# Kernel tuning notes

Hardware: AMD Instinct MI355X
Metric: run time of the kernel (lower is better)

Reference implementation:

```python
import jax, jax.numpy as jnp
import numpy as np

HEADS = 8
EPS = 1e-5
PW1 = (512, 8, 14, 14)   # (C, T, H, W), C = headsize1 * heads
PW2 = (512, 32, 7, 7)


def _ln(x, g, b):
    m = jnp.mean(x, axis=-1, keepdims=True)
    v = jnp.var(x, axis=-1, keepdims=True)
    return (x - m) * jax.lax.rsqrt(v + EPS) * g + b


def _mha(q, k, v):
    b, nq, c = q.shape
    nk = k.shape[1]
    hd = c // HEADS
    qh = q.reshape(b, nq, HEADS, hd).transpose(0, 2, 1, 3)  # [b,h,nq,hd]
    kh = k.reshape(b, nk, HEADS, hd).transpose(0, 2, 1, 3)
    vh = v.reshape(b, nk, HEADS, hd).transpose(0, 2, 1, 3)
    s = jnp.einsum('bhqd,bhkd->bhqk', qh, kh) * (hd ** -0.5)
    a = jax.nn.softmax(s, axis=-1)
    o = jnp.einsum('bhqk,bhkd->bhqd', a, vh)
    return o.transpose(0, 2, 1, 3).reshape(b, nq, c)


def _tok(x):
    b, c, t, h, w = x.shape
    return x.transpose(0, 2, 3, 4, 1).reshape(b, t * h * w, c)


def _detok(t, c, T, H, W):
    b = t.shape[0]
    return t.reshape(b, T, H, W, c).transpose(0, 4, 1, 2, 3)


def _out_head(y, w, bias, bn_g, bn_b):
    # 1x1x1 Conv3d + ReLU + BatchNorm3d (eval, running mean 0 / var 1)
    z = jnp.einsum('bcthw,oc->bothw', y, w) + bias[None, :, None, None, None]
    z = jax.nn.relu(z)
    z = z * jax.lax.rsqrt(jnp.float32(1.0 + EPS))
    return z * bn_g[None, :, None, None, None] + bn_b[None, :, None, None, None]


def reference(x1, x2, Wq1, bq1, Wk1, bk1, Wv1, bv1, ln1_g, ln1_b,
              Wq2, bq2, Wk2, bk2, Wv2, bv2, ln2_g, ln2_b,
              out1_w, out1_b, bn1_g, bn1_b, out2_w, out2_b, bn2_g, bn2_b):
    t1 = _tok(x1)  # [B, 1568, 512]
    t2 = _tok(x2)  # [B, 1568, 512]
    for i in range(3):  # three chained norm + cross-attn stages
        q1 = _ln(t1, ln1_g[i], ln1_b[i]) @ Wq1[i].T + bq1[i]
        k1 = t2 @ Wk1[i].T + bk1[i]
        v1 = t2 @ Wv1[i].T + bv1[i]
        q2 = _ln(t2, ln2_g[i], ln2_b[i]) @ Wq2[i].T + bq2[i]
        k2 = t1 @ Wk2[i].T + bk2[i]
        v2 = t1 @ Wv2[i].T + bv2[i]
        t1 = t1 + _mha(q1, k1, v1)
        t2 = t2 + _mha(q2, k2, v2)
    y1 = _detok(t1, *PW1)
    y2 = _detok(t2, *PW2)
    z1 = _out_head(y1, out1_w, out1_b, bn1_g, bn1_b)
    z2 = _out_head(y2, out2_w, out2_b, bn2_g, bn2_b)
    return (z1, z2)


def setup_inputs() -> dict:
    key = jax.random.key(0)
    ks = jax.random.split(key, 12)
    C = 512
    w = lambda k, shp: jax.random.normal(k, shp, jnp.float32) * 0.02
    return {
        'x1': jax.random.normal(ks[0], (4, C, 8, 14, 14), jnp.float32),
        'x2': jax.random.normal(ks[1], (4, C, 32, 7, 7), jnp.float32),
        'Wq1': w(ks[2], (3, C, C)), 'bq1': jnp.zeros((3, C), jnp.float32),
        'Wk1': w(ks[3], (3, C, C)), 'bk1': jnp.zeros((3, C), jnp.float32),
        'Wv1': w(ks[4], (3, C, C)), 'bv1': jnp.zeros((3, C), jnp.float32),
        'ln1_g': jnp.ones((3, C), jnp.float32), 'ln1_b': jnp.zeros((3, C), jnp.float32),
        'Wq2': w(ks[5], (3, C, C)), 'bq2': jnp.zeros((3, C), jnp.float32),
        'Wk2': w(ks[6], (3, C, C)), 'bk2': jnp.zeros((3, C), jnp.float32),
        'Wv2': w(ks[7], (3, C, C)), 'bv2': jnp.zeros((3, C), jnp.float32),
        'ln2_g': jnp.ones((3, C), jnp.float32), 'ln2_b': jnp.zeros((3, C), jnp.float32),
        'out1_w': w(ks[8], (C, C)), 'out1_b': jnp.zeros((C,), jnp.float32),
        'bn1_g': jnp.ones((C,), jnp.float32), 'bn1_b': jnp.zeros((C,), jnp.float32),
        'out2_w': w(ks[9], (C, C)), 'out2_b': jnp.zeros((C,), jnp.float32),
        'bn2_g': jnp.ones((C,), jnp.float32), 'bn2_b': jnp.zeros((C,), jnp.float32),
    }
```

## Files before the change

kernel.cpp:

```cpp
#include <hip/hip_runtime.h>

typedef __bf16 bf16_t;
typedef __bf16 bf16x8 __attribute__((ext_vector_type(8)));
typedef __bf16 bf16x4 __attribute__((ext_vector_type(4)));
typedef float f32x4 __attribute__((ext_vector_type(4)));
typedef float f32x16 __attribute__((ext_vector_type(16)));
typedef unsigned u32x4 __attribute__((ext_vector_type(4)));

#define NTOK 1568
#define CDIM 512
#define BATCH 4
#define MROWS (BATCH*NTOK)
#define RSQ1PEPS 0.9999950000374997f
#define CEXP 0.1803368801111204f
#define DEFER_THR 44.3614195558365f

__device__ __forceinline__ float fexp2(float x) {
  float r;
  asm("v_exp_f32 %0, %1" : "=v"(r) : "v"(x));
  return r;
}

struct CastArgs { const float* s[20]; };
__global__ __launch_bounds__(256) void cast_kernel(CastArgs ca, bf16_t* __restrict__ out) {
  int idx = blockIdx.x * 256 + threadIdx.x;
  int m = idx >> 16;
  const float4* sp = (const float4*)ca.s[m];
  float4 v = sp[idx & 65535];
  bf16x4 o;
  o[0] = (bf16_t)v.x; o[1] = (bf16_t)v.y; o[2] = (bf16_t)v.z; o[3] = (bf16_t)v.w;
  *(bf16x4*)(out + (size_t)idx * 4) = o;
}

struct TokArgs { const float* x[2]; float* tf[2]; bf16_t* tb[2]; };
__global__ __launch_bounds__(256) void tok_kernel(TokArgs ta) {
  __shared__ float tile[32][33];
  int z = blockIdx.z, sel = z >> 2, b = z & 3;
  int c0 = blockIdx.y * 32, s0 = blockIdx.x * 32;
  int tx = threadIdx.x, ty = threadIdx.y;
  const float* xp = ta.x[sel] + (size_t)b * CDIM * NTOK;
  for (int r = 0; r < 32; r += 8)
    tile[ty + r][tx] = xp[(size_t)(c0 + ty + r) * NTOK + s0 + tx];
  __syncthreads();
  float* tfp = ta.tf[sel] + (size_t)b * NTOK * CDIM;
  bf16_t* tbp = ta.tb[sel] + (size_t)b * NTOK * CDIM;
  for (int r = 0; r < 32; r += 8) {
    float v = tile[tx][ty + r];
    size_t idx = (size_t)(s0 + ty + r) * CDIM + c0 + tx;
    tfp[idx] = v;
    tbp[idx] = (bf16_t)v;
  }
}

__global__ __launch_bounds__(64) void ln_kernel(
    const float* __restrict__ t1, const float* __restrict__ t2,
    const float* __restrict__ g1, const float* __restrict__ b1,
    const float* __restrict__ g2, const float* __restrict__ b2,
    bf16_t* __restrict__ o1, bf16_t* __restrict__ o2) {
  int row = blockIdx.x;
  const float* t; const float* g; const float* bt; bf16_t* out;
  if (row < MROWS) { t = t1; g = g1; bt = b1; out = o1; }
  else { row -= MROWS; t = t2; g = g2; bt = b2; out = o2; }
  int l = threadIdx.x;
  const float* x = t + (size_t)row * CDIM;
  float4 v0 = ((const float4*)x)[l];
  float4 v1 = ((const float4*)x)[l + 64];
  float s = v0.x + v0.y + v0.z + v0.w + v1.x + v1.y + v1.z + v1.w;
  float sq = v0.x*v0.x + v0.y*v0.y + v0.z*v0.z + v0.w*v0.w
           + v1.x*v1.x + v1.y*v1.y + v1.z*v1.z + v1.w*v1.w;
  for (int m = 1; m < 64; m <<= 1) { s += __shfl_xor(s, m); sq += __shfl_xor(sq, m); }
  float mean = s * (1.f / 512.f);
  float var = sq * (1.f / 512.f) - mean * mean;
  float rs = rsqrtf(var + 1e-5f);
  float4 g0 = ((const float4*)g)[l], g1v = ((const float4*)g)[l + 64];
  float4 b0 = ((const float4*)bt)[l], b1v = ((const float4*)bt)[l + 64];
  bf16x4 o0, o1v;
  o0[0] = (bf16_t)((v0.x - mean) * rs * g0.x + b0.x);
  o0[1] = (bf16_t)((v0.y - mean) * rs * g0.y + b0.y);
  o0[2] = (bf16_t)((v0.z - mean) * rs * g0.z + b0.z);
  o0[3] = (bf16_t)((v0.w - mean) * rs * g0.w + b0.w);
  o1v[0] = (bf16_t)((v1.x - mean) * rs * g1v.x + b1v.x);
  o1v[1] = (bf16_t)((v1.y - mean) * rs * g1v.y + b1v.y);
  o1v[2] = (bf16_t)((v1.z - mean) * rs * g1v.z + b1v.z);
  o1v[3] = (bf16_t)((v1.w - mean) * rs * g1v.w + b1v.w);
  *(bf16x4*)(out + (size_t)row * CDIM + l * 4) = o0;
  *(bf16x4*)(out + (size_t)row * CDIM + 256 + l * 4) = o1v;
}

template<int MODE>
__device__ __forceinline__ void gemm_core(
    bf16_t (* __restrict__ As)[40], bf16_t (* __restrict__ Bs)[40],
    const bf16_t* __restrict__ A, const bf16_t* __restrict__ Bp,
    const float* __restrict__ bias, const float* __restrict__ bng,
    const float* __restrict__ bnb, bf16_t* __restrict__ outb,
    float* __restrict__ outf, int m0, int n0, int Nvalid) {
  int tid = threadIdx.x;
  int w = tid >> 6, l = tid & 63, lr = l & 15, kg = l >> 4;
  int wm = (w >> 1) * 64, wn = (w & 1) * 64;
  f32x4 acc[4][4];
  for (int i = 0; i < 4; i++)
    for (int j = 0; j < 4; j++)
      acc[i][j] = f32x4{0.f, 0.f, 0.f, 0.f};
  int srow = tid >> 1;
  int soff = (tid & 1) * 16;
  int brow = n0 + srow;
  if (MODE != 0 && brow >= Nvalid) brow = Nvalid - 1;
  const bf16_t* aq = A + (size_t)(m0 + srow) * CDIM + soff;
  const bf16_t* bq = Bp + (size_t)brow * CDIM + soff;
  for (int kk = 0; kk < 16; kk++) {
    __syncthreads();
    bf16x8 a0 = *(const bf16x8*)(aq);
    bf16x8 a1 = *(const bf16x8*)(aq + 8);
    bf16x8 b0 = *(const bf16x8*)(bq);
    bf16x8 b1 = *(const bf16x8*)(bq + 8);
    aq += 32; bq += 32;
    *(bf16x8*)&As[srow][soff] = a0;
    *(bf16x8*)&As[srow][soff + 8] = a1;
    *(bf16x8*)&Bs[srow][soff] = b0;
    *(bf16x8*)&Bs[srow][soff + 8] = b1;
    __syncthreads();
    bf16x8 af[4], bfr[4];
    for (int i = 0; i < 4; i++) af[i] = *(const bf16x8*)&As[wm + i * 16 + lr][kg * 8];
    for (int j = 0; j < 4; j++) bfr[j] = *(const bf16x8*)&Bs[wn + j * 16 + lr][kg * 8];
    for (int i = 0; i < 4; i++)
      for (int j = 0; j < 4; j++)
        acc[i][j] = __builtin_amdgcn_mfma_f32_16x16x32_bf16(af[i], bfr[j], acc[i][j], 0, 0, 0);
  }
  for (int i = 0; i < 4; i++)
    for (int j = 0; j < 4; j++) {
      int rbase = m0 + wm + i * 16 + kg * 4;
      int col = n0 + wn + j * 16 + lr;
      for (int r = 0; r < 4; r++) {
        int row = rbase + r;
        float v = acc[i][j][r];
        if (MODE == 0) {
          v += bias[col];
          outb[(size_t)row * CDIM + col] = (bf16_t)v;
        } else if (MODE == 1) {
          v += bias[row];
          v = v > 0.f ? v : 0.f;
          v *= RSQ1PEPS;
          v = v * bng[row] + bnb[row];
          if (col < Nvalid) outf[(size_t)row * NTOK + col] = v;
        } else {
          v += bias[row];
          if (col < Nvalid) outb[(size_t)row * NTOK + col] = (bf16_t)v;
        }
      }
    }
}

struct ProjArgs {
  const bf16_t* A0[4]; const bf16_t* W0[4]; const float* b0[4]; bf16_t* o0[4];
  const bf16_t* W2[2]; const bf16_t* B2[2]; const float* b2[2]; bf16_t* o2[2];
};
__global__ __launch_bounds__(256) void proj_kernel(ProjArgs p) {
  __shared__ bf16_t As[128][40];
  __shared__ bf16_t Bs[128][40];
  int id = blockIdx.x;
  if (id < 784) {
    int set = id / 196, rem = id % 196;
    int n0 = (rem & 3) * 128, m0 = (rem >> 2) * 128;
    gemm_core<0>(As, Bs, p.A0[set], p.W0[set], p.b0[set], nullptr, nullptr,
                 p.o0[set], nullptr, m0, n0, 512);
  } else {
    int j = id - 784;
    int unit = j / 52;
    int which = unit >> 2, bat = unit & 3;
    int rem = j % 52;
    int n0 = (rem % 13) * 128, m0 = (rem / 13) * 128;
    gemm_core<2>(As, Bs, p.W2[which], p.B2[which] + (size_t)bat * NTOK * CDIM,
                 p.b2[which], nullptr, nullptr,
                 p.o2[which] + (size_t)bat * CDIM * NTOK, nullptr, m0, n0, NTOK);
  }
}

__global__ __launch_bounds__(256) void head_kernel(
    const bf16_t* __restrict__ W1, const bf16_t* __restrict__ W2,
    const bf16_t* __restrict__ t1b, const bf16_t* __restrict__ t2b,
    const float* __restrict__ b1, const float* __restrict__ b2,
    const float* __restrict__ bng1, const float* __restrict__ bnb1,
    const float* __restrict__ bng2, const float* __restrict__ bnb2,
    float* __restrict__ out) {
  __shared__ bf16_t As[128][40];
  __shared__ bf16_t Bs[128][40];
  int z = blockIdx.z;
  int which = z >> 2, bat = z & 3;
  const bf16_t* A = which ? W2 : W1;
  const bf16_t* Bp = (which ? t2b : t1b) + (size_t)bat * NTOK * CDIM;
  const float* bias = which ? b2 : b1;
  const float* bng = which ? bng2 : bng1;
  const float* bnb = which ? bnb2 : bnb1;
  float* outf = out + (size_t)which * BATCH * CDIM * NTOK + (size_t)bat * CDIM * NTOK;
  int m0 = blockIdx.y * 128, n0 = blockIdx.x * 128;
  gemm_core<1>(As, Bs, A, Bp, bias, bng, bnb, nullptr, outf, m0, n0, NTOK);
}

__device__ __forceinline__ void attn_tile(
    const bf16_t* __restrict__ Ksl, const bf16_t* __restrict__ Vsl,
    const bf16x8* __restrict__ qf, int lo, int hi,
    float& m_i, float& l_i, f32x16& ot0, f32x16& ot1) {
  f32x16 st;
#pragma unroll
  for (int r = 0; r < 16; r++) st[r] = 0.f;
  __builtin_amdgcn_s_setprio(1);
#pragma unroll
  for (int c = 0; c < 4; c++) {
    bf16x8 kf = *(const bf16x8*)(Ksl + lo * 64 + ((c * 16 + hi * 8) ^ ((lo & 7) << 3)));
    st = __builtin_amdgcn_mfma_f32_32x32x16_bf16(kf, qf[c], st, 0, 0, 0);
  }
  __builtin_amdgcn_s_setprio(0);
  float a0 = fmaxf(st[0], st[1]), a1 = fmaxf(st[2], st[3]);
  float a2 = fmaxf(st[4], st[5]), a3 = fmaxf(st[6], st[7]);
  float a4 = fmaxf(st[8], st[9]), a5 = fmaxf(st[10], st[11]);
  float a6 = fmaxf(st[12], st[13]), a7 = fmaxf(st[14], st[15]);
  a0 = fmaxf(a0, a1); a2 = fmaxf(a2, a3); a4 = fmaxf(a4, a5); a6 = fmaxf(a6, a7);
  a0 = fmaxf(a0, a2); a4 = fmaxf(a4, a6);
  float tm = fmaxf(a0, a4);
  tm = fmaxf(tm, __shfl_xor(tm, 32));
  if (!__all(tm <= m_i + DEFER_THR)) {
    float mn = fmaxf(m_i, tm);
    float alpha = fexp2((m_i - mn) * CEXP);
#pragma unroll
    for (int r = 0; r < 16; r++) { ot0[r] *= alpha; ot1[r] *= alpha; }
    l_i *= alpha;
    m_i = mn;
  }
  float nmC = -m_i * CEXP;
  float p[16];
#pragma unroll
  for (int r = 0; r < 16; r++) p[r] = fexp2(fmaf(st[r], CEXP, nmC));
  float s0 = (p[0] + p[1]) + (p[2] + p[3]);
  float s1 = (p[4] + p[5]) + (p[6] + p[7]);
  float s2 = (p[8] + p[9]) + (p[10] + p[11]);
  float s3 = (p[12] + p[13]) + (p[14] + p[15]);
  float ts = (s0 + s1) + (s2 + s3);
  ts += __shfl_xor(ts, 32);
  l_i += ts;
  unsigned pk[8];
#pragma unroll
  for (int g = 0; g < 8; g++) {
    union { bf16_t hh[2]; unsigned u; } cv;
    cv.hh[0] = (bf16_t)p[2 * g];
    cv.hh[1] = (bf16_t)p[2 * g + 1];
    pk[g] = cv.u;
  }
  unsigned x0 = __shfl_xor((int)pk[0], 32), x1 = __shfl_xor((int)pk[1], 32);
  unsigned x2 = __shfl_xor((int)pk[2], 32), x3 = __shfl_xor((int)pk[3], 32);
  unsigned x4 = __shfl_xor((int)pk[4], 32), x5 = __shfl_xor((int)pk[5], 32);
  unsigned x6 = __shfl_xor((int)pk[6], 32), x7 = __shfl_xor((int)pk[7], 32);
  union { u32x4 u; bf16x8 bv; } F0, F1;
  F0.u[0] = hi ? x2 : pk[0];
  F0.u[1] = hi ? x3 : pk[1];
  F0.u[2] = hi ? pk[2] : x0;
  F0.u[3] = hi ? pk[3] : x1;
  F1.u[0] = hi ? x6 : pk[4];
  F1.u[1] = hi ? x7 : pk[5];
  F1.u[2] = hi ? pk[6] : x4;
  F1.u[3] = hi ? pk[7] : x5;
  __builtin_amdgcn_s_setprio(1);
  {
    bf16x8 v0 = *(const bf16x8*)(Vsl + lo * 40 + hi * 8);
    ot0 = __builtin_amdgcn_mfma_f32_32x32x16_bf16(v0, F0.bv, ot0, 0, 0, 0);
    bf16x8 v1 = *(const bf16x8*)(Vsl + lo * 40 + 16 + hi * 8);
    ot0 = __builtin_amdgcn_mfma_f32_32x32x16_bf16(v1, F1.bv, ot0, 0, 0, 0);
    bf16x8 v2 = *(const bf16x8*)(Vsl + (32 + lo) * 40 + hi * 8);
    ot1 = __builtin_amdgcn_mfma_f32_32x32x16_bf16(v2, F0.bv, ot1, 0, 0, 0);
    bf16x8 v3 = *(const bf16x8*)(Vsl + (32 + lo) * 40 + 16 + hi * 8);
    ot1 = __builtin_amdgcn_mfma_f32_32x32x16_bf16(v3, F1.bv, ot1, 0, 0, 0);
  }
  __builtin_amdgcn_s_setprio(0);
}

struct AttnArgs {
  const bf16_t* q[2]; const bf16_t* k[2]; const bf16_t* v[2];
  float* tf[2]; bf16_t* tb[2];
};

#define ATTN_STEP(TT, CUR, WSLOT, ISLOT, VLOAD, VSTORE)                              \
  {                                                                                  \
    int ktn = (TT) + 2 > 48 ? 48 : (TT) + 2;                                         \
    __builtin_amdgcn_global_load_lds(                                                \
        (const __attribute__((address_space(1))) unsigned*)(kgl + (size_t)ktn * 32 * CDIM), \
        (__attribute__((address_space(3))) unsigned*)&Ks[ISLOT][w * 8][0], 16, 0, 0); \
    VLOAD = *(const bf16x8*)(vgl + ktn * 32);                                        \
    attn_tile(&Ks[CUR][0][0], &Vs[CUR][0][0], qf, lo, hi, m_i, l_i, ot0, ot1);       \
    asm volatile("s_waitcnt vmcnt(2)" ::: "memory");                                 \
    *(bf16x8*)&Vs[WSLOT][vd][vc] = VSTORE;                                           \
    asm volatile("s_waitcnt lgkmcnt(0)\n\ts_barrier" ::: "memory");                  \
  }

__global__ __launch_bounds__(256) void attn_kernel(AttnArgs aa) {
  __shared__ alignas(16) bf16_t Ks[4][32][64];
  __shared__ alignas(16) bf16_t Vs[4][64][40];
  int id = blockIdx.x;
  int xcd = id & 7, sl = id >> 3;
  int g = xcd + ((sl / 13) << 3);
  int qt = sl % 13;
  int ss = g >> 5, b = (g >> 3) & 3, h = g & 7;
  const bf16_t* qg = aa.q[ss];
  const bf16_t* kgp = aa.k[ss];
  const bf16_t* vtg = aa.v[ss];
  float* tf = aa.tf[ss];
  bf16_t* tb = aa.tb[ss];
  int tid = threadIdx.x, w = tid >> 6, l = tid & 63;
  int lo = l & 31, hi = l >> 5;
  const size_t kbase = ((size_t)b * NTOK) * CDIM + h * 64;
  const size_t vbase = ((size_t)b * CDIM + h * 64) * NTOK;

  int q0 = qt * 128 + w * 32;
  int qrow = q0 + lo;
  int qr = qrow < NTOK ? qrow : NTOK - 1;
  const bf16_t* qp = qg + kbase + (size_t)qr * CDIM + hi * 8;
  bf16x8 qf[4];
  qf[0] = *(const bf16x8*)(qp);
  qf[1] = *(const bf16x8*)(qp + 16);
  qf[2] = *(const bf16x8*)(qp + 32);
  qf[3] = *(const bf16x8*)(qp + 48);
  asm volatile("" : "+v"(qf[0]), "+v"(qf[1]), "+v"(qf[2]), "+v"(qf[3]));
  asm volatile("s_waitcnt vmcnt(0)" ::: "memory");

  int ksr = w * 8 + (l >> 3);
  int ksc = 8 * ((l & 7) ^ ((l >> 3) & 7));
  const bf16_t* kgl = kgp + kbase + (size_t)ksr * CDIM + ksc;
  int vd = tid >> 2, vc = (tid & 3) * 8;
  const bf16_t* vgl = vtg + vbase + (size_t)vd * NTOK + vc;

  float m_i = -3.0e38f, l_i = 0.f;
  f32x16 ot0, ot1;
#pragma unroll
  for (int r = 0; r < 16; r++) { ot0[r] = 0.f; ot1[r] = 0.f; }

  bf16x8 vrA, vrB;
  __builtin_amdgcn_global_load_lds(
      (const __attribute__((address_space(1))) unsigned*)(kgl),
      (__attribute__((address_space(3))) unsigned*)&Ks[0][w * 8][0], 16, 0, 0);
  vrB = *(const bf16x8*)(vgl);
  __builtin_amdgcn_global_load_lds(
      (const __attribute__((address_space(1))) unsigned*)(kgl + (size_t)32 * CDIM),
      (__attribute__((address_space(3))) unsigned*)&Ks[1][w * 8][0], 16, 0, 0);
  vrA = *(const bf16x8*)(vgl + 32);
  asm volatile("s_waitcnt vmcnt(2)" ::: "memory");
  *(bf16x8*)&Vs[0][vd][vc] = vrB;
  asm volatile("s_waitcnt lgkmcnt(0)\n\ts_barrier" ::: "memory");

  for (int t = 0; t < 48; t += 4) {
    ATTN_STEP(t + 0, 0, 1, 2, vrB, vrA);
    ATTN_STEP(t + 1, 1, 2, 3, vrA, vrB);
    ATTN_STEP(t + 2, 2, 3, 0, vrB, vrA);
    ATTN_STEP(t + 3, 3, 0, 1, vrA, vrB);
  }
  attn_tile(&Ks[0][0][0], &Vs[0][0][0], qf, lo, hi, m_i, l_i, ot0, ot1);
  asm volatile("s_waitcnt vmcnt(0)" ::: "memory");

  if (qrow < NTOK) {
    float inv = 1.f / l_i;
    float* tfp = tf + ((size_t)b * NTOK + qrow) * CDIM + h * 64 + hi * 4;
    bf16_t* tbp = tb + ((size_t)b * NTOK + qrow) * CDIM + h * 64 + hi * 4;
#pragma unroll
    for (int db = 0; db < 2; db++) {
#pragma unroll
      for (int gq = 0; gq < 4; gq++) {
        int doff = db * 32 + gq * 8;
        float4 old = *(float4*)(tfp + doff);
        float4 nv;
        float a0 = (db ? ot1[gq * 4 + 0] : ot0[gq * 4 + 0]) * inv;
        float a1 = (db ? ot1[gq * 4 + 1] : ot0[gq * 4 + 1]) * inv;
        float a2 = (db ? ot1[gq * 4 + 2] : ot0[gq * 4 + 2]) * inv;
        float a3 = (db ? ot1[gq * 4 + 3] : ot0[gq * 4 + 3]) * inv;
        nv.x = old.x + a0; nv.y = old.y + a1; nv.z = old.z + a2; nv.w = old.w + a3;
        *(float4*)(tfp + doff) = nv;
        bf16x4 ob;
        ob[0] = (bf16_t)nv.x; ob[1] = (bf16_t)nv.y;
        ob[2] = (bf16_t)nv.z; ob[3] = (bf16_t)nv.w;
        *(bf16x4*)(tbp + doff) = ob;
      }
    }
  }
}

extern "C" void kernel_launch(void* const* d_in, const int* in_sizes, int n_in,
                              void* d_out, int out_size, void* d_ws, size_t ws_size,
                              hipStream_t stream) {
  (void)in_sizes; (void)n_in; (void)out_size; (void)ws_size;
  const float* x1 = (const float*)d_in[0];
  const float* x2 = (const float*)d_in[1];
  const float* Wq1 = (const float*)d_in[2];
  const float* bq1 = (const float*)d_in[3];
  const float* Wk1 = (const float*)d_in[4];
  const float* bk1 = (const float*)d_in[5];
  const float* Wv1 = (const float*)d_in[6];
  const float* bv1 = (const float*)d_in[7];
  const float* ln1_g = (const float*)d_in[8];
  const float* ln1_b = (const float*)d_in[9];
  const float* Wq2 = (const float*)d_in[10];
  const float* bq2 = (const float*)d_in[11];
  const float* Wk2 = (const float*)d_in[12];
  const float* bk2 = (const float*)d_in[13];
  const float* Wv2 = (const float*)d_in[14];
  const float* bv2 = (const float*)d_in[15];
  const float* ln2_g = (const float*)d_in[16];
  const float* ln2_b = (const float*)d_in[17];
  const float* out1_w = (const float*)d_in[18];
  const float* out1_b = (const float*)d_in[19];
  const float* bn1_g = (const float*)d_in[20];
  const float* bn1_b = (const float*)d_in[21];
  const float* out2_w = (const float*)d_in[22];
  const float* out2_b = (const float*)d_in[23];
  const float* bn2_g = (const float*)d_in[24];
  const float* bn2_b = (const float*)d_in[25];

  const size_t WMAT = 512 * 512;
  char* ws = (char*)d_ws;
  bf16_t* wb = (bf16_t*)ws;
  size_t off = 20 * WMAT * sizeof(bf16_t);
  float* t1f = (float*)(ws + off); off += (size_t)MROWS * CDIM * 4;
  float* t2f = (float*)(ws + off); off += (size_t)MROWS * CDIM * 4;
  bf16_t* t1b = (bf16_t*)(ws + off); off += (size_t)MROWS * CDIM * 2;
  bf16_t* t2b = (bf16_t*)(ws + off); off += (size_t)MROWS * CDIM * 2;
  bf16_t* l1b = (bf16_t*)(ws + off); off += (size_t)MROWS * CDIM * 2;
  bf16_t* l2b = (bf16_t*)(ws + off); off += (size_t)MROWS * CDIM * 2;
  bf16_t* q1b = (bf16_t*)(ws + off); off += (size_t)MROWS * CDIM * 2;
  bf16_t* k1b = (bf16_t*)(ws + off); off += (size_t)MROWS * CDIM * 2;
  bf16_t* v1b = (bf16_t*)(ws + off); off += (size_t)MROWS * CDIM * 2;
  bf16_t* q2b = (bf16_t*)(ws + off); off += (size_t)MROWS * CDIM * 2;
  bf16_t* k2b = (bf16_t*)(ws + off); off += (size_t)MROWS * CDIM * 2;
  bf16_t* v2b = (bf16_t*)(ws + off); off += (size_t)MROWS * CDIM * 2;

  CastArgs ca;
  for (int i = 0; i < 3; i++) {
    ca.s[0 + i] = Wq1 + (size_t)i * WMAT;
    ca.s[3 + i] = Wk1 + (size_t)i * WMAT;
    ca.s[6 + i] = Wv1 + (size_t)i * WMAT;
    ca.s[9 + i] = Wq2 + (size_t)i * WMAT;
    ca.s[12 + i] = Wk2 + (size_t)i * WMAT;
    ca.s[15 + i] = Wv2 + (size_t)i * WMAT;
  }
  ca.s[18] = out1_w;
  ca.s[19] = out2_w;
  cast_kernel<<<5120, 256, 0, stream>>>(ca, wb);

  TokArgs ta;
  ta.x[0] = x1; ta.x[1] = x2;
  ta.tf[0] = t1f; ta.tf[1] = t2f;
  ta.tb[0] = t1b; ta.tb[1] = t2b;
  tok_kernel<<<dim3(49, 16, 8), dim3(32, 8), 0, stream>>>(ta);

  AttnArgs aa;
  aa.q[0] = q1b; aa.q[1] = q2b;
  aa.k[0] = k1b; aa.k[1] = k2b;
  aa.v[0] = v1b; aa.v[1] = v2b;
  aa.tf[0] = t1f; aa.tf[1] = t2f;
  aa.tb[0] = t1b; aa.tb[1] = t2b;

  for (int i = 0; i < 3; i++) {
    ln_kernel<<<2 * MROWS, 64, 0, stream>>>(t1f, t2f,
        ln1_g + i * 512, ln1_b + i * 512, ln2_g + i * 512, ln2_b + i * 512,
        l1b, l2b);
    ProjArgs pa;
    pa.A0[0] = l1b; pa.W0[0] = wb + (0 + i) * WMAT; pa.b0[0] = bq1 + i * 512; pa.o0[0] = q1b;
    pa.A0[1] = t2b; pa.W0[1] = wb + (3 + i) * WMAT; pa.b0[1] = bk1 + i * 512; pa.o0[1] = k1b;
    pa.A0[2] = l2b; pa.W0[2] = wb + (9 + i) * WMAT; pa.b0[2] = bq2 + i * 512; pa.o0[2] = q2b;
    pa.A0[3] = t1b; pa.W0[3] = wb + (12 + i) * WMAT; pa.b0[3] = bk2 + i * 512; pa.o0[3] = k2b;
    pa.W2[0] = wb + (6 + i) * WMAT; pa.B2[0] = t2b; pa.b2[0] = bv1 + i * 512; pa.o2[0] = v1b;
    pa.W2[1] = wb + (15 + i) * WMAT; pa.B2[1] = t1b; pa.b2[1] = bv2 + i * 512; pa.o2[1] = v2b;
    proj_kernel<<<1200, 256, 0, stream>>>(pa);
    attn_kernel<<<832, 256, 0, stream>>>(aa);
  }

  float* out = (float*)d_out;
  head_kernel<<<dim3(13, 4, 8), 256, 0, stream>>>(
      wb + 18 * WMAT, wb + 19 * WMAT, t1b, t2b,
      out1_b, out2_b, bn1_g, bn1_b, bn2_g, bn2_b, out);
}
```

Measured before the change: 487.4 us.

## Process 64-key attention tiles with triple-buffered direct-to-LDS K and V loads

The attention inner loop now handles 64 keys per step instead of 32, halving the number of barriers and pipeline steps, and uses a 3-slot ring buffer in place of 4 slots. V is now loaded straight into LDS with global_load_lds and an XOR swizzle, removing the register staging and separate LDS store. The cross-half P fragment exchange uses v_permlane32_swap in place of eight shuffles. The cost is more live registers per step (two score accumulators) and a special tail tile.

```diff
diff --git a/kernel.cpp b/kernel.cpp
--- a/kernel.cpp
+++ b/kernel.cpp
@@ -19,6 +19,12 @@
   float r;
   asm("v_exp_f32 %0, %1" : "=v"(r) : "v"(x));
   return r;
+}
+
+__device__ __forceinline__ void glds16(const bf16_t* src, bf16_t* dst) {
+  __builtin_amdgcn_global_load_lds(
+      (const __attribute__((address_space(1))) unsigned*)src,
+      (__attribute__((address_space(3))) unsigned*)dst, 16, 0, 0);
 }
 
 struct CastArgs { const float* s[20]; };
@@ -196,47 +202,16 @@
   gemm_core<1>(As, Bs, A, Bp, bias, bng, bnb, nullptr, outf, m0, n0, NTOK);
 }
 
-__device__ __forceinline__ void attn_tile(
-    const bf16_t* __restrict__ Ksl, const bf16_t* __restrict__ Vsl,
-    const bf16x8* __restrict__ qf, int lo, int hi,
-    float& m_i, float& l_i, f32x16& ot0, f32x16& ot1) {
-  f32x16 st;
-#pragma unroll
-  for (int r = 0; r < 16; r++) st[r] = 0.f;
-  __builtin_amdgcn_s_setprio(1);
-#pragma unroll
-  for (int c = 0; c < 4; c++) {
-    bf16x8 kf = *(const bf16x8*)(Ksl + lo * 64 + ((c * 16 + hi * 8) ^ ((lo & 7) << 3)));
-    st = __builtin_amdgcn_mfma_f32_32x32x16_bf16(kf, qf[c], st, 0, 0, 0);
-  }
-  __builtin_amdgcn_s_setprio(0);
-  float a0 = fmaxf(st[0], st[1]), a1 = fmaxf(st[2], st[3]);
-  float a2 = fmaxf(st[4], st[5]), a3 = fmaxf(st[6], st[7]);
-  float a4 = fmaxf(st[8], st[9]), a5 = fmaxf(st[10], st[11]);
-  float a6 = fmaxf(st[12], st[13]), a7 = fmaxf(st[14], st[15]);
+__device__ __forceinline__ float tree_max16(const f32x16& s) {
+  float a0 = fmaxf(s[0], s[1]), a1 = fmaxf(s[2], s[3]);
+  float a2 = fmaxf(s[4], s[5]), a3 = fmaxf(s[6], s[7]);
+  float a4 = fmaxf(s[8], s[9]), a5 = fmaxf(s[10], s[11]);
+  float a6 = fmaxf(s[12], s[13]), a7 = fmaxf(s[14], s[15]);
   a0 = fmaxf(a0, a1); a2 = fmaxf(a2, a3); a4 = fmaxf(a4, a5); a6 = fmaxf(a6, a7);
-  a0 = fmaxf(a0, a2); a4 = fmaxf(a4, a6);
-  float tm = fmaxf(a0, a4);
-  tm = fmaxf(tm, __shfl_xor(tm, 32));
-  if (!__all(tm <= m_i + DEFER_THR)) {
-    float mn = fmaxf(m_i, tm);
-    float alpha = fexp2((m_i - mn) * CEXP);
-#pragma unroll
-    for (int r = 0; r < 16; r++) { ot0[r] *= alpha; ot1[r] *= alpha; }
-    l_i *= alpha;
-    m_i = mn;
-  }
-  float nmC = -m_i * CEXP;
-  float p[16];
-#pragma unroll
-  for (int r = 0; r < 16; r++) p[r] = fexp2(fmaf(st[r], CEXP, nmC));
-  float s0 = (p[0] + p[1]) + (p[2] + p[3]);
-  float s1 = (p[4] + p[5]) + (p[6] + p[7]);
-  float s2 = (p[8] + p[9]) + (p[10] + p[11]);
-  float s3 = (p[12] + p[13]) + (p[14] + p[15]);
-  float ts = (s0 + s1) + (s2 + s3);
-  ts += __shfl_xor(ts, 32);
-  l_i += ts;
+  return fmaxf(fmaxf(a0, a2), fmaxf(a4, a6));
+}
+
+__device__ __forceinline__ void build_frags(const float* p, bf16x8& Fa, bf16x8& Fb) {
   unsigned pk[8];
 #pragma unroll
   for (int g = 0; g < 8; g++) {
@@ -245,29 +220,101 @@
     cv.hh[1] = (bf16_t)p[2 * g + 1];
     pk[g] = cv.u;
   }
-  unsigned x0 = __shfl_xor((int)pk[0], 32), x1 = __shfl_xor((int)pk[1], 32);
-  unsigned x2 = __shfl_xor((int)pk[2], 32), x3 = __shfl_xor((int)pk[3], 32);
-  unsigned x4 = __shfl_xor((int)pk[4], 32), x5 = __shfl_xor((int)pk[5], 32);
-  unsigned x6 = __shfl_xor((int)pk[6], 32), x7 = __shfl_xor((int)pk[7], 32);
-  union { u32x4 u; bf16x8 bv; } F0, F1;
-  F0.u[0] = hi ? x2 : pk[0];
-  F0.u[1] = hi ? x3 : pk[1];
-  F0.u[2] = hi ? pk[2] : x0;
-  F0.u[3] = hi ? pk[3] : x1;
-  F1.u[0] = hi ? x6 : pk[4];
-  F1.u[1] = hi ? x7 : pk[5];
-  F1.u[2] = hi ? pk[6] : x4;
-  F1.u[3] = hi ? pk[7] : x5;
+  asm volatile("v_permlane32_swap_b32 %0, %1" : "+v"(pk[0]), "+v"(pk[2]));
+  asm volatile("v_permlane32_swap_b32 %0, %1" : "+v"(pk[1]), "+v"(pk[3]));
+  asm volatile("v_permlane32_swap_b32 %0, %1" : "+v"(pk[4]), "+v"(pk[6]));
+  asm volatile("v_permlane32_swap_b32 %0, %1" : "+v"(pk[5]), "+v"(pk[7]));
+  union { u32x4 u; bf16x8 bv; } A, B;
+  A.u[0] = pk[0]; A.u[1] = pk[1]; A.u[2] = pk[2]; A.u[3] = pk[3];
+  B.u[0] = pk[4]; B.u[1] = pk[5]; B.u[2] = pk[6]; B.u[3] = pk[7];
+  Fa = A.bv; Fb = B.bv;
+}
+
+template<bool TAIL>
+__device__ __forceinline__ void attn_tile64(
+    const bf16_t* __restrict__ Ksl, const bf16_t* __restrict__ Vsl,
+    const bf16x8* __restrict__ qf, const f32x16& z, int lo, int hi,
+    float& m_i, float& l_i, f32x16& ot0, f32x16& ot1) {
+  int sw = (lo & 7) << 3;
+  f32x16 sa, sb;
   __builtin_amdgcn_s_setprio(1);
   {
-    bf16x8 v0 = *(const bf16x8*)(Vsl + lo * 40 + hi * 8);
-    ot0 = __builtin_amdgcn_mfma_f32_32x32x16_bf16(v0, F0.bv, ot0, 0, 0, 0);
-    bf16x8 v1 = *(const bf16x8*)(Vsl + lo * 40 + 16 + hi * 8);
-    ot0 = __builtin_amdgcn_mfma_f32_32x32x16_bf16(v1, F1.bv, ot0, 0, 0, 0);
-    bf16x8 v2 = *(const bf16x8*)(Vsl + (32 + lo) * 40 + hi * 8);
-    ot1 = __builtin_amdgcn_mfma_f32_32x32x16_bf16(v2, F0.bv, ot1, 0, 0, 0);
-    bf16x8 v3 = *(const bf16x8*)(Vsl + (32 + lo) * 40 + 16 + hi * 8);
-    ot1 = __builtin_amdgcn_mfma_f32_32x32x16_bf16(v3, F1.bv, ot1, 0, 0, 0);
+    const bf16_t* kr = Ksl + lo * 64;
+    bf16x8 k0 = *(const bf16x8*)(kr + ((hi * 8) ^ sw));
+    sa = __builtin_amdgcn_mfma_f32_32x32x16_bf16(k0, qf[0], z, 0, 0, 0);
+    bf16x8 k1 = *(const bf16x8*)(kr + ((16 + hi * 8) ^ sw));
+    sa = __builtin_amdgcn_mfma_f32_32x32x16_bf16(k1, qf[1], sa, 0, 0, 0);
+    bf16x8 k2 = *(const bf16x8*)(kr + ((32 + hi * 8) ^ sw));
+    sa = __builtin_amdgcn_mfma_f32_32x32x16_bf16(k2, qf[2], sa, 0, 0, 0);
+    bf16x8 k3 = *(const bf16x8*)(kr + ((48 + hi * 8) ^ sw));
+    sa = __builtin_amdgcn_mfma_f32_32x32x16_bf16(k3, qf[3], sa, 0, 0, 0);
+  }
+  if (!TAIL) {
+    const bf16_t* kr = Ksl + (32 + lo) * 64;
+    bf16x8 k0 = *(const bf16x8*)(kr + ((hi * 8) ^ sw));
+    sb = __builtin_amdgcn_mfma_f32_32x32x16_bf16(k0, qf[0], z, 0, 0, 0);
+    bf16x8 k1 = *(const bf16x8*)(kr + ((16 + hi * 8) ^ sw));
+    sb = __builtin_amdgcn_mfma_f32_32x32x16_bf16(k1, qf[1], sb, 0, 0, 0);
+    bf16x8 k2 = *(const bf16x8*)(kr + ((32 + hi * 8) ^ sw));
+    sb = __builtin_amdgcn_mfma_f32_32x32x16_bf16(k2, qf[2], sb, 0, 0, 0);
+    bf16x8 k3 = *(const bf16x8*)(kr + ((48 + hi * 8) ^ sw));
+    sb = __builtin_amdgcn_mfma_f32_32x32x16_bf16(k3, qf[3], sb, 0, 0, 0);
+  }
+  __builtin_amdgcn_s_setprio(0);
+  float tm = tree_max16(sa);
+  if (!TAIL) tm = fmaxf(tm, tree_max16(sb));
+  tm = fmaxf(tm, __shfl_xor(tm, 32));
+  if (!__all(tm <= m_i + DEFER_THR)) {
+    float mn = fmaxf(m_i, tm);
+    float alpha = fexp2((m_i - mn) * CEXP);
+#pragma unroll
+    for (int r = 0; r < 16; r++) { ot0[r] *= alpha; ot1[r] *= alpha; }
+    l_i *= alpha;
+    m_i = mn;
+  }
+  float nmC = -m_i * CEXP;
+  float pa[16], pb[16];
+#pragma unroll
+  for (int r = 0; r < 16; r++) pa[r] = fexp2(fmaf(sa[r], CEXP, nmC));
+  float ts = ((pa[0] + pa[1]) + (pa[2] + pa[3])) + ((pa[4] + pa[5]) + (pa[6] + pa[7]))
+           + ((pa[8] + pa[9]) + (pa[10] + pa[11])) + ((pa[12] + pa[13]) + (pa[14] + pa[15]));
+  if (!TAIL) {
+#pragma unroll
+    for (int r = 0; r < 16; r++) pb[r] = fexp2(fmaf(sb[r], CEXP, nmC));
+    ts += ((pb[0] + pb[1]) + (pb[2] + pb[3])) + ((pb[4] + pb[5]) + (pb[6] + pb[7]))
+        + ((pb[8] + pb[9]) + (pb[10] + pb[11])) + ((pb[12] + pb[13]) + (pb[14] + pb[15]));
+  }
+  ts += __shfl_xor(ts, 32);
+  l_i += ts;
+  bf16x8 F0, F1, F2, F3;
+  build_frags(pa, F0, F1);
+  if (!TAIL) build_frags(pb, F2, F3);
+  __builtin_amdgcn_s_setprio(1);
+  {
+    const bf16_t* vr = Vsl + lo * 64;
+    bf16x8 v0 = *(const bf16x8*)(vr + ((hi * 8) ^ sw));
+    ot0 = __builtin_amdgcn_mfma_f32_32x32x16_bf16(v0, F0, ot0, 0, 0, 0);
+    bf16x8 v1 = *(const bf16x8*)(vr + ((16 + hi * 8) ^ sw));
+    ot0 = __builtin_amdgcn_mfma_f32_32x32x16_bf16(v1, F1, ot0, 0, 0, 0);
+    if (!TAIL) {
+      bf16x8 v2 = *(const bf16x8*)(vr + ((32 + hi * 8) ^ sw));
+      ot0 = __builtin_amdgcn_mfma_f32_32x32x16_bf16(v2, F2, ot0, 0, 0, 0);
+      bf16x8 v3 = *(const bf16x8*)(vr + ((48 + hi * 8) ^ sw));
+      ot0 = __builtin_amdgcn_mfma_f32_32x32x16_bf16(v3, F3, ot0, 0, 0, 0);
+    }
+  }
+  {
+    const bf16_t* vr = Vsl + (32 + lo) * 64;
+    bf16x8 v0 = *(const bf16x8*)(vr + ((hi * 8) ^ sw));
+    ot1 = __builtin_amdgcn_mfma_f32_32x32x16_bf16(v0, F0, ot1, 0, 0, 0);
+    bf16x8 v1 = *(const bf16x8*)(vr + ((16 + hi * 8) ^ sw));
+    ot1 = __builtin_amdgcn_mfma_f32_32x32x16_bf16(v1, F1, ot1, 0, 0, 0);
+    if (!TAIL) {
+      bf16x8 v2 = *(const bf16x8*)(vr + ((32 + hi * 8) ^ sw));
+      ot1 = __builtin_amdgcn_mfma_f32_32x32x16_bf16(v2, F2, ot1, 0, 0, 0);
+      bf16x8 v3 = *(const bf16x8*)(vr + ((48 + hi * 8) ^ sw));
+      ot1 = __builtin_amdgcn_mfma_f32_32x32x16_bf16(v3, F3, ot1, 0, 0, 0);
+    }
   }
   __builtin_amdgcn_s_setprio(0);
 }
@@ -277,22 +324,32 @@
   float* tf[2]; bf16_t* tb[2];
 };
 
-#define ATTN_STEP(TT, CUR, WSLOT, ISLOT, VLOAD, VSTORE)                              \
-  {                                                                                  \
-    int ktn = (TT) + 2 > 48 ? 48 : (TT) + 2;                                         \
-    __builtin_amdgcn_global_load_lds(                                                \
-        (const __attribute__((address_space(1))) unsigned*)(kgl + (size_t)ktn * 32 * CDIM), \
-        (__attribute__((address_space(3))) unsigned*)&Ks[ISLOT][w * 8][0], 16, 0, 0); \
-    VLOAD = *(const bf16x8*)(vgl + ktn * 32);                                        \
-    attn_tile(&Ks[CUR][0][0], &Vs[CUR][0][0], qf, lo, hi, m_i, l_i, ot0, ot1);       \
-    asm volatile("s_waitcnt vmcnt(2)" ::: "memory");                                 \
-    *(bf16x8*)&Vs[WSLOT][vd][vc] = VSTORE;                                           \
-    asm volatile("s_waitcnt lgkmcnt(0)\n\ts_barrier" ::: "memory");                  \
+#define STAGE(TN, SL)                                                         \
+  {                                                                           \
+    int tnS_ = (TN);                                                          \
+    const bf16_t* k0 = kgl + (size_t)tnS_ * (64 * CDIM);                      \
+    const bf16_t* k1 = (tnS_ == 24) ? (kgl + (size_t)1536 * CDIM)             \
+                                    : (k0 + (size_t)32 * CDIM);               \
+    const bf16_t* v0 = (tnS_ == 24) ? vglT : (vgl + tnS_ * 64);               \
+    glds16(k0, &Ks[SL][wq8][0]);                                              \
+    glds16(k1, &Ks[SL][32 + wq8][0]);                                         \
+    glds16(v0, &Vs[SL][wq8][0]);                                              \
+    glds16(v0 + (size_t)32 * NTOK, &Vs[SL][32 + wq8][0]);                     \
+  }
+
+#define ATTN_STEP(TT, CUR, NXT)                                               \
+  {                                                                           \
+    int tn_ = (TT) + 2; if (tn_ > 24) tn_ = 24;                               \
+    STAGE(tn_, NXT);                                                          \
+    attn_tile64<false>(&Ks[CUR][0][0], &Vs[CUR][0][0], qf, z, lo, hi,         \
+                       m_i, l_i, ot0, ot1);                                   \
+    asm volatile("s_waitcnt vmcnt(4)" ::: "memory");                          \
+    __builtin_amdgcn_s_barrier();                                             \
   }
 
 __global__ __launch_bounds__(256) void attn_kernel(AttnArgs aa) {
-  __shared__ alignas(16) bf16_t Ks[4][32][64];
-  __shared__ alignas(16) bf16_t Vs[4][64][40];
+  __shared__ alignas(16) bf16_t Ks[3][64][64];
+  __shared__ alignas(16) bf16_t Vs[3][64][64];
   int id = blockIdx.x;
   int xcd = id & 7, sl = id >> 3;
   int g = xcd + ((sl / 13) << 3);
@@ -305,6 +362,7 @@
   bf16_t* tb = aa.tb[ss];
   int tid = threadIdx.x, w = tid >> 6, l = tid & 63;
   int lo = l & 31, hi = l >> 5;
+  int wq8 = w * 8;
   const size_t kbase = ((size_t)b * NTOK) * CDIM + h * 64;
   const size_t vbase = ((size_t)b * CDIM + h * 64) * NTOK;
 
@@ -320,37 +378,29 @@
   asm volatile("" : "+v"(qf[0]), "+v"(qf[1]), "+v"(qf[2]), "+v"(qf[3]));
   asm volatile("s_waitcnt vmcnt(0)" ::: "memory");
 
-  int ksr = w * 8 + (l >> 3);
-  int ksc = 8 * ((l & 7) ^ ((l >> 3) & 7));
-  const bf16_t* kgl = kgp + kbase + (size_t)ksr * CDIM + ksc;
-  int vd = tid >> 2, vc = (tid & 3) * 8;
-  const bf16_t* vgl = vtg + vbase + (size_t)vd * NTOK + vc;
+  int row0 = wq8 + (l >> 3);
+  int slotx = (l & 7) ^ ((l >> 3) & 7);
+  const bf16_t* kgl = kgp + kbase + (size_t)row0 * CDIM + slotx * 8;
+  const bf16_t* vgl = vtg + vbase + (size_t)row0 * NTOK + slotx * 8;
+  int kcT = 1536 + slotx * 8; if (kcT > 1560) kcT = 1560;
+  const bf16_t* vglT = vtg + vbase + (size_t)row0 * NTOK + kcT;
 
   float m_i = -3.0e38f, l_i = 0.f;
-  f32x16 ot0, ot1;
-#pragma unroll
-  for (int r = 0; r < 16; r++) { ot0[r] = 0.f; ot1[r] = 0.f; }
-
-  bf16x8 vrA, vrB;
-  __builtin_amdgcn_global_load_lds(
-      (const __attribute__((address_space(1))) unsigned*)(kgl),
-      (__attribute__((address_space(3))) unsigned*)&Ks[0][w * 8][0], 16, 0, 0);
-  vrB = *(const bf16x8*)(vgl);
-  __builtin_amdgcn_global_load_lds(
-      (const __attribute__((address_space(1))) unsigned*)(kgl + (size_t)32 * CDIM),
-      (__attribute__((address_space(3))) unsigned*)&Ks[1][w * 8][0], 16, 0, 0);
-  vrA = *(const bf16x8*)(vgl + 32);
-  asm volatile("s_waitcnt vmcnt(2)" ::: "memory");
-  *(bf16x8*)&Vs[0][vd][vc] = vrB;
-  asm volatile("s_waitcnt lgkmcnt(0)\n\ts_barrier" ::: "memory");
-
-  for (int t = 0; t < 48; t += 4) {
-    ATTN_STEP(t + 0, 0, 1, 2, vrB, vrA);
-    ATTN_STEP(t + 1, 1, 2, 3, vrA, vrB);
-    ATTN_STEP(t + 2, 2, 3, 0, vrB, vrA);
-    ATTN_STEP(t + 3, 3, 0, 1, vrA, vrB);
-  }
-  attn_tile(&Ks[0][0][0], &Vs[0][0][0], qf, lo, hi, m_i, l_i, ot0, ot1);
+  f32x16 ot0, ot1, z;
+#pragma unroll
+  for (int r = 0; r < 16; r++) { ot0[r] = 0.f; ot1[r] = 0.f; z[r] = 0.f; }
+
+  STAGE(0, 0);
+  STAGE(1, 1);
+  asm volatile("s_waitcnt vmcnt(4)" ::: "memory");
+  __builtin_amdgcn_s_barrier();
+
+  for (int t = 0; t < 24; t += 3) {
+    ATTN_STEP(t + 0, 0, 2);
+    ATTN_STEP(t + 1, 1, 0);
+    ATTN_STEP(t + 2, 2, 1);
+  }
+  attn_tile64<true>(&Ks[0][0][0], &Vs[0][0][0], qf, z, lo, hi, m_i, l_i, ot0, ot1);
   asm volatile("s_waitcnt vmcnt(0)" ::: "memory");
 
   if (qrow < NTOK) {
```

Result: faster. 452.3 us (-7.2%).
